# Kernel optimization log

Measured on AMD Instinct MI355X. Metric: run time of the kernel, lower is better.

The kernel has to match this reference:

```python
import jax, jax.numpy as jnp
import numpy as np

# Static dims
N = 512        # nodes
T = 8          # window_size
E = 16384      # edges per timestep
F0, H1, FP = 128, 256, 64   # feat_proj_dims
FN = 16        # noise dim
WIN = FP + FN  # WLE in_channels = 80
WH = 128       # WLE hidden
D_SSM = 1      # TLSSM d_model = d_ssm = 1 (scalar per node pair)
D_STATE = 16
D_CONV = 4
CONV_DIM = D_SSM + 2 * D_STATE          # 33
D_IN = 2 * D_SSM + 2 * D_STATE + 1      # z, xBC, dt -> 35
PRED = 1


def setup_inputs() -> dict:
    key = jax.random.key(0)
    ks = jax.random.split(key, 24)
    s = 0.05
    rn = lambda k, shp: jax.random.normal(k, shp, dtype=jnp.float32) * s
    return {
        "edge_index": jax.random.randint(ks[0], (T, 2, E), 0, N, dtype=jnp.int64),
        "edge_weight": jax.random.uniform(ks[1], (T, E), dtype=jnp.float32),
        "feats": jax.random.normal(ks[2], (T, N, F0), dtype=jnp.float32),
        "noise": jax.random.normal(ks[3], (T, N, FN), dtype=jnp.float32),
        # feat_proj MLP
        "Wp1": rn(ks[4], (F0, H1)), "bp1": jnp.zeros((H1,), jnp.float32),
        "Wp2": rn(ks[5], (H1, FP)), "bp2": jnp.zeros((FP,), jnp.float32),
        # WeightedLinkEncoder
        "wle_W1": rn(ks[6], (WIN, WH)), "wle_b1": jnp.zeros((WH,), jnp.float32),
        "wle_W2": rn(ks[7], (WH, WH)), "wle_b2": jnp.zeros((WH,), jnp.float32),
        "wle_W3": rn(ks[8], (WH, WH)), "wle_b3": jnp.zeros((WH,), jnp.float32),
        "wle_w4": rn(ks[9], (WH, 1)), "wle_b4": jnp.zeros((1,), jnp.float32),
        # TLSSM (Mamba2-style stepwise)
        "W_in": rn(ks[10], (D_SSM, D_IN)),
        "conv_w": rn(ks[11], (CONV_DIM, D_CONV)),
        "conv_b": jnp.zeros((CONV_DIM,), jnp.float32),
        "dt_bias": jnp.zeros((1,), jnp.float32),
        "A_log": jnp.zeros((1,), jnp.float32),
        "D_skip": jnp.ones((1,), jnp.float32) * s,
        "W_out": rn(ks[12], (D_SSM, D_SSM)),
    }


def _forward(edge_index, edge_weight, feats, noise,
             Wp1, bp1, Wp2, bp2,
             wle_W1, wle_b1, wle_W2, wle_b2, wle_W3, wle_b3, wle_w4, wle_b4,
             W_in, conv_w, conv_b, dt_bias, A_log, D_skip, W_out):
    # feat_proj: stacked Linear+ReLU, vectorized over timesteps
    h = jax.nn.relu(feats @ Wp1 + bp1)
    h = jax.nn.relu(h @ Wp2 + bp2)              # [T, N, FP]
    emb = jnp.concatenate([h, noise], axis=-1)

    # WeightedLinkEncoder: node MLP -> weighted sparse propagation -> edge score
    def wle(x, ei, ew):
        hh = jax.nn.relu(x @ wle_W1 + wle_b1)                       # [N, WH]
        msg = ew[:, None] * hh[ei[1]]                               # gather neighbors
        agg = jax.ops.segment_sum(msg, ei[0], num_segments=N)      # scatter-add
        h2 = jax.nn.relu((hh + agg) @ wle_W2 + wle_b2)
        ef = h2[ei[0]] * h2[ei[1]]                                 # per-edge hadamard
        s = jax.nn.relu(ef @ wle_W3 + wle_b3) @ wle_w4 + wle_b4    # [E, 1]
        return s[:, 0]

    scores = jax.vmap(wle)(emb, edge_index, edge_weight)            # [T, E]

    # SparseTensor(...).to_dense(): densify edge scores to N x N per step
    def dens(ei, s):
        return jnp.zeros((N, N), scores.dtype).at[ei[0], ei[1]].set(s)

    dense = jax.vmap(dens)(edge_index, scores).reshape(T, N * N, D_SSM)

    # TLSSM stepwise recurrence over the window, batch = N*N
    A = -jnp.exp(A_log)  # [1]

    def step(carry, xt):
        conv_state, ssm_state = carry                    # [BN,CONV_DIM,D_CONV], [BN,D_SSM,D_STATE]
        zxbcdt = xt @ W_in                               # [BN, D_IN]
        z, xBC, dt = jnp.split(zxbcdt, [D_SSM, D_SSM + CONV_DIM], axis=-1)
        conv_state = jnp.concatenate([conv_state[:, :, 1:], xBC[:, :, None]], axis=-1)
        xBC = jax.nn.silu(jnp.sum(conv_state * conv_w, axis=-1) + conv_b)
        x_, Bm, Cm = jnp.split(xBC, [D_SSM, D_SSM + D_STATE], axis=-1)
        dt = jax.nn.softplus(dt + dt_bias)               # [BN, 1]
        dA = jnp.exp(dt * A)                             # [BN, 1]
        ssm_state = ssm_state * dA[:, :, None] + (dt * x_)[:, :, None] * Bm[:, None, :]
        y = jnp.sum(ssm_state * Cm[:, None, :], axis=-1) + D_skip * x_
        y = y * jax.nn.silu(z)
        return (conv_state, ssm_state), y @ W_out

    conv0 = jnp.zeros((N * N, CONV_DIM, D_CONV), jnp.float32)
    ssm0 = jnp.zeros((N * N, D_SSM, D_STATE), jnp.float32)
    _, ys = jax.lax.scan(step, (conv0, ssm0), dense)     # [T, BN, 1]
    out = ys.reshape(T, N, N)[-PRED:]                    # pred_flag=True: last pred_size steps
    return out


def reference(edge_index, edge_weight, feats, noise,
              Wp1, bp1, Wp2, bp2,
              wle_W1, wle_b1, wle_W2, wle_b2, wle_W3, wle_b3, wle_w4, wle_b4,
              W_in, conv_w, conv_b, dt_bias, A_log, D_skip, W_out):
    return _forward(edge_index, edge_weight, feats, noise,
                    Wp1, bp1, Wp2, bp2,
                    wle_W1, wle_b1, wle_W2, wle_b2, wle_W3, wle_b3, wle_w4, wle_b4,
                    W_in, conv_w, conv_b, dt_bias, A_log, D_skip, W_out)
```

## Files before the change

### kernel.cpp

```cpp
#include <hip/hip_runtime.h>
#include <math.h>

#define Nn 512
#define Tt 8
#define Ee 16384
#define NNc (Nn*Nn)
#define TNr (Tt*Nn)
#define TE  (Tt*Ee)
#define CAP 128

typedef __bf16 bf16x8 __attribute__((ext_vector_type(8)));
typedef float  f32x4  __attribute__((ext_vector_type(4)));
union BU { uint4 q; bf16x8 v; };

__device__ __forceinline__ void dec2(float x0, float x1, unsigned &hi, unsigned &lo){
    unsigned u0 = __float_as_uint(x0), u1 = __float_as_uint(x1);
    unsigned t0 = u0 + 0x7FFFu + ((u0>>16)&1u);
    unsigned t1 = u1 + 0x7FFFu + ((u1>>16)&1u);
    hi = (t0>>16) | (t1 & 0xFFFF0000u);
    float h0 = __uint_as_float(t0 & 0xFFFF0000u);
    float h1 = __uint_as_float(t1 & 0xFFFF0000u);
    float l0 = x0 - h0, l1 = x1 - h1;
    unsigned v0 = __float_as_uint(l0), v1 = __float_as_uint(l1);
    unsigned s0 = v0 + 0x7FFFu + ((v0>>16)&1u);
    unsigned s1 = v1 + 0x7FFFu + ((v1>>16)&1u);
    lo = (s0>>16) | (s1 & 0xFFFF0000u);
}

__global__ __launch_bounds__(256) void k_pf(
    const int* __restrict__ ei, const float* __restrict__ W3,
    unsigned short* __restrict__ w3h, unsigned short* __restrict__ w3l,
    int* __restrict__ cnt, int* __restrict__ tag, float4* __restrict__ out4,
    const float* __restrict__ feats, const float* __restrict__ noise,
    const float* __restrict__ Wp1, const float* __restrict__ bp1,
    const float* __restrict__ Wp2, const float* __restrict__ bp2,
    const float* __restrict__ W1, const float* __restrict__ b1,
    float* __restrict__ hh)
{
    __shared__ float sh1[8][256];
    __shared__ float semb[8][80];
    int tid = threadIdx.x;
    if (blockIdx.x < 64){
        int e = blockIdx.x*256 + tid;
        int a = ei[7*2*Ee + e], b = ei[7*2*Ee + Ee + e];
        int cell = a*Nn + b;
#pragma unroll
        for (int t=0;t<8;++t) tag[t*NNc + cell] = 0;
        if (e < TNr) cnt[e] = 0;
        float4 z = {0.f,0.f,0.f,0.f};
#pragma unroll
        for (int q=0;q<4;++q) out4[q*16384 + e] = z;
        int i    = e & 7;
        int lane = (e>>3) & 63;
        int jt   = (e>>9) & 7;
        int kt   = e>>12;
        int k = kt*32 + (lane>>4)*8 + i;
        int j = jt*16 + (lane&15);
        float x = W3[k*128 + j];
        unsigned u = __float_as_uint(x);
        unsigned t = u + 0x7FFFu + ((u>>16)&1u);
        w3h[e] = (unsigned short)(t>>16);
        float hf = __uint_as_float(t & 0xFFFF0000u);
        float lf = x - hf;
        unsigned v = __float_as_uint(lf);
        unsigned s = v + 0x7FFFu + ((v>>16)&1u);
        w3l[e] = (unsigned short)(s>>16);
        return;
    }
    int r0 = (blockIdx.x - 64) * 8;
    if (tid < 128){
        int r = tid>>4, k = tid&15;
        semb[r][64+k] = noise[(size_t)(r0+r)*16 + k];
    }
    {
        const float* __restrict__ fr = &feats[(size_t)r0*128];
        float acc[8];
#pragma unroll
        for (int r=0;r<8;++r) acc[r]=0.f;
#pragma unroll 2
        for (int i=0;i<128;i+=4){
            float w0=Wp1[(i+0)*256+tid], w1=Wp1[(i+1)*256+tid];
            float w2=Wp1[(i+2)*256+tid], w3=Wp1[(i+3)*256+tid];
#pragma unroll
            for (int r=0;r<8;++r){
                float4 f = *(const float4*)&fr[r*128 + i];
                acc[r] += f.x*w0 + f.y*w1 + f.z*w2 + f.w*w3;
            }
        }
        float b = bp1[tid];
#pragma unroll
        for (int r=0;r<8;++r) sh1[r][tid] = fmaxf(acc[r]+b, 0.f);
    }
    __syncthreads();
    {
        int jo = tid & 63, rq = tid >> 6;
        float a0=0.f, a1=0.f;
#pragma unroll 2
        for (int i=0;i<256;i+=4){
            float w0=Wp2[(i+0)*64+jo], w1=Wp2[(i+1)*64+jo];
            float w2=Wp2[(i+2)*64+jo], w3=Wp2[(i+3)*64+jo];
            float4 f0 = *(const float4*)&sh1[rq][i];
            float4 f1 = *(const float4*)&sh1[rq+4][i];
            a0 += f0.x*w0 + f0.y*w1 + f0.z*w2 + f0.w*w3;
            a1 += f1.x*w0 + f1.y*w1 + f1.z*w2 + f1.w*w3;
        }
        float b = bp2[jo];
        semb[rq][jo]   = fmaxf(a0+b, 0.f);
        semb[rq+4][jo] = fmaxf(a1+b, 0.f);
    }
    __syncthreads();
    {
        int j = tid & 127, rh = tid >> 7;
        float a[4];
#pragma unroll
        for (int q=0;q<4;++q) a[q]=0.f;
#pragma unroll 2
        for (int i=0;i<80;i+=4){
            float w0=W1[(i+0)*128+j], w1=W1[(i+1)*128+j];
            float w2=W1[(i+2)*128+j], w3=W1[(i+3)*128+j];
#pragma unroll
            for (int q=0;q<4;++q){
                float4 f = *(const float4*)&semb[rh+2*q][i];
                a[q] += f.x*w0 + f.y*w1 + f.z*w2 + f.w*w3;
            }
        }
        float b = b1[j];
#pragma unroll
        for (int q=0;q<4;++q)
            hh[(size_t)(r0+rh+2*q)*128 + j] = fmaxf(a[q]+b, 0.f);
    }
}

__global__ __launch_bounds__(256) void k_histtag(
    const int* __restrict__ ei, const float* __restrict__ ew,
    int* __restrict__ cnt, int2* __restrict__ bucket2, int* __restrict__ tag)
{
    int g = blockIdx.x*256 + threadIdx.x;
    int t = g>>14, e = g&(Ee-1);
    int a = ei[t*2*Ee + e];
    int b = ei[t*2*Ee + Ee + e];
    int cell = t*Nn + a;
    int pos = atomicAdd(&cnt[cell], 1);
    if (pos < CAP) bucket2[(size_t)cell*CAP + pos] = make_int2(b, __float_as_int(ew[g]));
    atomicMax(&tag[t*NNc + a*Nn + b], g+1);
}

__global__ __launch_bounds__(256) void k_sw(
    const float* __restrict__ hh, const int* __restrict__ cnt,
    const int2* __restrict__ bucket2,
    const float* __restrict__ W2, const float* __restrict__ b2,
    float* __restrict__ h2)
{
    __shared__ float sx[2][128];
    int dloc = threadIdx.x >> 7;
    int ch = threadIdx.x & 127;
    int bidd = blockIdx.x*2 + dloc;
    int t = bidd >> 9;
    int n = cnt[bidd]; n = n < CAP ? n : CAP;
    const int2* __restrict__ bk = &bucket2[(size_t)bidd*CAP];
    const float* __restrict__ hht = &hh[(size_t)t*Nn*128];
    float acc = hh[(size_t)bidd*128 + ch];
    int i = 0;
    for (; i+1 < n; i += 2){
        int2 p0 = bk[i], p1 = bk[i+1];
        acc += __int_as_float(p0.y)*hht[(size_t)p0.x*128 + ch]
             + __int_as_float(p1.y)*hht[(size_t)p1.x*128 + ch];
    }
    if (i < n){
        int2 p = bk[i];
        acc += __int_as_float(p.y)*hht[(size_t)p.x*128 + ch];
    }
    sx[dloc][ch] = acc;
    __syncthreads();
    float s = 0.f;
    for (int i2=0; i2<128; i2+=4){
        float4 x = *(const float4*)&sx[dloc][i2];
        s += x.x*W2[(i2+0)*128+ch] + x.y*W2[(i2+1)*128+ch]
           + x.z*W2[(i2+2)*128+ch] + x.w*W2[(i2+3)*128+ch];
    }
    h2[(size_t)bidd*128 + ch] = fmaxf(s + b2[ch], 0.f);
}

__global__ __launch_bounds__(512) void k_edge9(
    const int* __restrict__ ei, const float* __restrict__ h2,
    const uint4* __restrict__ w3h, const uint4* __restrict__ w3l,
    const float* __restrict__ b3, const float* __restrict__ w4,
    const float* __restrict__ b4, float* __restrict__ sc)
{
    __shared__ uint4 sBh[2048];
    __shared__ uint4 sBl[2048];
    int tid = threadIdx.x;
    int bid = blockIdx.x;
#pragma unroll
    for (int q=0;q<4;++q){
        sBh[q*512+tid] = w3h[q*512+tid];
        sBl[q*512+tid] = w3l[q*512+tid];
    }
    int tb  = bid >> 6;
    int e0b = (bid & 63) * 256;
    int w   = tid >> 6, lane = tid & 63;
    int e0w = e0b + w*32;
    int r16 = lane & 15, g4 = lane >> 4;

    const int* __restrict__ eit = &ei[tb*2*Ee];
    int a0 = eit[e0w + r16],      s0 = eit[Ee + e0w + r16];
    int a1 = eit[e0w + 16 + r16], s1 = eit[Ee + e0w + 16 + r16];
    const float* __restrict__ pa0 = &h2[(size_t)(tb*Nn+a0)*128];
    const float* __restrict__ pb0 = &h2[(size_t)(tb*Nn+s0)*128];
    const float* __restrict__ pa1 = &h2[(size_t)(tb*Nn+a1)*128];
    const float* __restrict__ pb1 = &h2[(size_t)(tb*Nn+s1)*128];

    f32x4 acc0[8], acc1[8];
#pragma unroll
    for (int jt=0;jt<8;++jt){
        acc0[jt] = (f32x4){0.f,0.f,0.f,0.f};
        acc1[jt] = (f32x4){0.f,0.f,0.f,0.f};
    }

    float4 rA0,rA1,rB0,rB1,rC0,rC1,rD0,rD1;
#define LOADK(kt) { int k0=(kt)*32+g4*8; \
    rA0=*(const float4*)&pa0[k0]; rA1=*(const float4*)&pa0[k0+4]; \
    rB0=*(const float4*)&pb0[k0]; rB1=*(const float4*)&pb0[k0+4]; \
    rC0=*(const float4*)&pa1[k0]; rC1=*(const float4*)&pa1[k0+4]; \
    rD0=*(const float4*)&pb1[k0]; rD1=*(const float4*)&pb1[k0+4]; }

    BU ah0[2], al0[2], ah1[2], al1[2];
#define DECK(s) { uint4 hq,lq; \
    dec2(rA0.x*rB0.x, rA0.y*rB0.y, hq.x, lq.x); \
    dec2(rA0.z*rB0.z, rA0.w*rB0.w, hq.y, lq.y); \
    dec2(rA1.x*rB1.x, rA1.y*rB1.y, hq.z, lq.z); \
    dec2(rA1.z*rB1.z, rA1.w*rB1.w, hq.w, lq.w); \
    ah0[s].q=hq; al0[s].q=lq; \
    dec2(rC0.x*rD0.x, rC0.y*rD0.y, hq.x, lq.x); \
    dec2(rC0.z*rD0.z, rC0.w*rD0.w, hq.y, lq.y); \
    dec2(rC1.x*rD1.x, rC1.y*rD1.y, hq.z, lq.z); \
    dec2(rC1.z*rD1.z, rC1.w*rD1.w, hq.w, lq.w); \
    ah1[s].q=hq; al1[s].q=lq; }

    LOADK(0)
    DECK(0)
    __syncthreads();
#pragma unroll
    for (int kt=0;kt<4;++kt){
        if (kt < 3) LOADK(kt+1)
        const int s = kt & 1;
#pragma unroll
        for (int jt=0;jt<8;++jt){
            BU Bh, Bl;
            Bh.q = sBh[(kt*8+jt)*64 + lane];
            Bl.q = sBl[(kt*8+jt)*64 + lane];
            acc0[jt] = __builtin_amdgcn_mfma_f32_16x16x32_bf16(ah0[s].v, Bh.v, acc0[jt], 0,0,0);
            acc0[jt] = __builtin_amdgcn_mfma_f32_16x16x32_bf16(ah0[s].v, Bl.v, acc0[jt], 0,0,0);
            acc0[jt] = __builtin_amdgcn_mfma_f32_16x16x32_bf16(al0[s].v, Bh.v, acc0[jt], 0,0,0);
            acc1[jt] = __builtin_amdgcn_mfma_f32_16x16x32_bf16(ah1[s].v, Bh.v, acc1[jt], 0,0,0);
            acc1[jt] = __builtin_amdgcn_mfma_f32_16x16x32_bf16(ah1[s].v, Bl.v, acc1[jt], 0,0,0);
            acc1[jt] = __builtin_amdgcn_mfma_f32_16x16x32_bf16(al1[s].v, Bh.v, acc1[jt], 0,0,0);
        }
        if (kt < 3) DECK((kt+1)&1)
    }

    float b4v = b4[0];
    float b3v[8], w4v[8];
#pragma unroll
    for (int jt=0;jt<8;++jt){ b3v[jt] = b3[jt*16 + r16]; w4v[jt] = w4[jt*16 + r16]; }
#pragma unroll
    for (int r=0;r<4;++r){
        float p0 = 0.f, p1 = 0.f;
#pragma unroll
        for (int jt=0;jt<8;++jt){
            p0 += fmaxf(acc0[jt][r] + b3v[jt], 0.f) * w4v[jt];
            p1 += fmaxf(acc1[jt][r] + b3v[jt], 0.f) * w4v[jt];
        }
        p0 += __shfl_xor(p0,1); p0 += __shfl_xor(p0,2);
        p0 += __shfl_xor(p0,4); p0 += __shfl_xor(p0,8);
        p1 += __shfl_xor(p1,1); p1 += __shfl_xor(p1,2);
        p1 += __shfl_xor(p1,4); p1 += __shfl_xor(p1,8);
        if (r16 == 0){
            sc[(size_t)tb*Ee + e0w + g4*4 + r]      = p0 + b4v;
            sc[(size_t)tb*Ee + e0w + 16 + g4*4 + r] = p1 + b4v;
        }
    }
}

__global__ __launch_bounds__(256) void k_ssm2(
    const int* __restrict__ ei, const int* __restrict__ tag,
    const float* __restrict__ sc,
    const float* __restrict__ W_in, const float* __restrict__ conv_w,
    const float* __restrict__ conv_b, const float* __restrict__ dt_bias,
    const float* __restrict__ A_log, const float* __restrict__ D_skip,
    const float* __restrict__ W_out, float* __restrict__ out)
{
    __shared__ float scw[132], scb[33], swin[35];
    int tid = threadIdx.x;
    if (tid < 132) scw[tid] = conv_w[tid];
    if (tid < 33)  scb[tid] = conv_b[tid];
    if (tid < 35)  swin[tid] = W_in[tid];
    __syncthreads();

    int e = blockIdx.x*256 + tid;
    int a = ei[7*2*Ee + e], b = ei[7*2*Ee + Ee + e];
    int cell = a*Nn + b;
    float x[8];
#pragma unroll
    for (int t=0;t<8;++t){
        int tg = tag[t*NNc + cell];
        x[t] = (tg > 0) ? sc[tg-1] : 0.f;
    }

    float A    = -expf(A_log[0]);
    float dtb  = dt_bias[0];
    float dsk  = D_skip[0];
    float wout = W_out[0];
    float win_z = swin[0], win_dt = swin[34];

    float ssm[16];
#pragma unroll
    for (int q=0;q<16;++q) ssm[q]=0.f;
    float h0=0.f,h1=0.f,h2v=0.f;
    float y=0.f;
    for (int t=0;t<8;++t){
        float xt = x[t];
        float act[33];
#pragma unroll
        for (int c=0;c<33;++c){
            float s = h0*scw[c*4+0] + h1*scw[c*4+1] + h2v*scw[c*4+2] + xt*scw[c*4+3];
            float pre = swin[1+c]*s + scb[c];
            act[c] = pre / (1.f + expf(-pre));
        }
        float x_ = act[0];
        float dtr = xt*win_dt + dtb;
        float dt  = (dtr > 20.f) ? dtr : log1pf(expf(dtr));
        float dA  = expf(dt*A);
        float dx  = dt*x_;
        float yv = 0.f;
#pragma unroll
        for (int q=0;q<16;++q){
            ssm[q] = ssm[q]*dA + dx*act[1+q];
            yv += ssm[q]*act[17+q];
        }
        yv += dsk*x_;
        float z = xt*win_z;
        yv *= z / (1.f + expf(-z));
        y = yv;
        h0=h1; h1=h2v; h2v=xt;
    }
    out[cell] = y*wout;
}

extern "C" void kernel_launch(void* const* d_in, const int* in_sizes, int n_in,
                              void* d_out, int out_size, void* d_ws, size_t ws_size,
                              hipStream_t stream)
{
    const int*   ei    = (const int*)d_in[0];
    const float* ew    = (const float*)d_in[1];
    const float* feats = (const float*)d_in[2];
    const float* noise = (const float*)d_in[3];
    const float* Wp1=(const float*)d_in[4];  const float* bp1=(const float*)d_in[5];
    const float* Wp2=(const float*)d_in[6];  const float* bp2=(const float*)d_in[7];
    const float* W1 =(const float*)d_in[8];  const float* b1 =(const float*)d_in[9];
    const float* W2 =(const float*)d_in[10]; const float* b2 =(const float*)d_in[11];
    const float* W3 =(const float*)d_in[12]; const float* b3 =(const float*)d_in[13];
    const float* w4 =(const float*)d_in[14]; const float* b4 =(const float*)d_in[15];
    const float* W_in  =(const float*)d_in[16]; const float* conv_w=(const float*)d_in[17];
    const float* conv_b=(const float*)d_in[18]; const float* dt_bias=(const float*)d_in[19];
    const float* A_log =(const float*)d_in[20]; const float* D_skip=(const float*)d_in[21];
    const float* W_out =(const float*)d_in[22];

    float* out = (float*)d_out;
    float* ws  = (float*)d_ws;
    float* hh    = ws;
    float* h2    = hh    + 524288;
    float* sc    = h2    + 524288;
    int*   cnt   = (int*)(sc + 131072);
    int*   tag   = cnt + TNr;
    int2*  bucket2 = (int2*)(tag + 2097152);
    unsigned short* w3h = (unsigned short*)(bucket2 + (size_t)TNr*CAP);
    unsigned short* w3l = w3h + 16384;

    k_pf      <<<576, 256, 0, stream>>>(ei, W3, w3h, w3l, cnt, tag, (float4*)out,
                                        feats, noise, Wp1, bp1, Wp2, bp2, W1, b1, hh);
    k_histtag <<<TE/256, 256, 0, stream>>>(ei, ew, cnt, bucket2, tag);
    k_sw      <<<TNr/2, 256, 0, stream>>>(hh, cnt, bucket2, W2, b2, h2);
    k_edge9   <<<512, 512, 0, stream>>>(ei, h2, (const uint4*)w3h, (const uint4*)w3l,
                                        b3, w4, b4, sc);
    k_ssm2    <<<Ee/256, 256, 0, stream>>>(ei, tag, sc, W_in, conv_w, conv_b,
                                           dt_bias, A_log, D_skip, W_out, out);
}
```

Before: 105.4 us.

## Move first feature-projection layer onto split-bf16 MFMA in a separate kernel

The first projection layer (feats @ Wp1) leaves the fused per-8-row FMA kernel and becomes its own kernel. That kernel uses 16x16x32 bf16 MFMA with a hi/lo split (three MFMAs per tile) to keep near-fp32 accuracy. A prep kernel pre-splits Wp1 into MFMA-fragment-ordered bf16 halves, and the remaining layers run in a second kernel that reads h1 through the bucket workspace region. The aim is to replace the large scalar FMA cost, at the price of two extra launches, an h1 round trip through global memory, and a k_l1 grid of only 32 blocks.

Result: slower. 118.8 us (+12.6%).

```diff
diff --git a/kernel.cpp b/kernel.cpp
--- a/kernel.cpp
+++ b/kernel.cpp
@@ -27,18 +27,24 @@
     lo = (s0>>16) | (s1 & 0xFFFF0000u);
 }
 
-__global__ __launch_bounds__(256) void k_pf(
+__device__ __forceinline__ void splitw(float x, unsigned short* ph, unsigned short* pl, int idx){
+    unsigned u = __float_as_uint(x);
+    unsigned t = u + 0x7FFFu + ((u>>16)&1u);
+    ph[idx] = (unsigned short)(t>>16);
+    float hf = __uint_as_float(t & 0xFFFF0000u);
+    float lf = x - hf;
+    unsigned v = __float_as_uint(lf);
+    unsigned s = v + 0x7FFFu + ((v>>16)&1u);
+    pl[idx] = (unsigned short)(s>>16);
+}
+
+__global__ __launch_bounds__(256) void k_prep(
     const int* __restrict__ ei, const float* __restrict__ W3,
+    const float* __restrict__ Wp1,
     unsigned short* __restrict__ w3h, unsigned short* __restrict__ w3l,
-    int* __restrict__ cnt, int* __restrict__ tag, float4* __restrict__ out4,
-    const float* __restrict__ feats, const float* __restrict__ noise,
-    const float* __restrict__ Wp1, const float* __restrict__ bp1,
-    const float* __restrict__ Wp2, const float* __restrict__ bp2,
-    const float* __restrict__ W1, const float* __restrict__ b1,
-    float* __restrict__ hh)
-{
-    __shared__ float sh1[8][256];
-    __shared__ float semb[8][80];
+    unsigned short* __restrict__ p1h, unsigned short* __restrict__ p1l,
+    int* __restrict__ cnt, int* __restrict__ tag, float4* __restrict__ out4)
+{
     int tid = threadIdx.x;
     if (blockIdx.x < 64){
         int e = blockIdx.x*256 + tid;
@@ -56,40 +62,104 @@
         int kt   = e>>12;
         int k = kt*32 + (lane>>4)*8 + i;
         int j = jt*16 + (lane&15);
-        float x = W3[k*128 + j];
-        unsigned u = __float_as_uint(x);
-        unsigned t = u + 0x7FFFu + ((u>>16)&1u);
-        w3h[e] = (unsigned short)(t>>16);
-        float hf = __uint_as_float(t & 0xFFFF0000u);
-        float lf = x - hf;
-        unsigned v = __float_as_uint(lf);
-        unsigned s = v + 0x7FFFu + ((v>>16)&1u);
-        w3l[e] = (unsigned short)(s>>16);
+        splitw(W3[k*128 + j], w3h, w3l, e);
         return;
     }
-    int r0 = (blockIdx.x - 64) * 8;
+    int idx = (blockIdx.x - 64)*256 + tid;
+    int i    = idx & 7;
+    int lane = (idx>>3) & 63;
+    int jt   = (idx>>9) & 15;
+    int kt   = idx>>13;
+    int k = kt*32 + (lane>>4)*8 + i;
+    int j = jt*16 + (lane&15);
+    splitw(Wp1[k*256 + j], p1h, p1l, idx);
+}
+
+__global__ __launch_bounds__(256) void k_l1(
+    const float* __restrict__ feats, const uint4* __restrict__ p1h,
+    const uint4* __restrict__ p1l, const float* __restrict__ bp1,
+    float* __restrict__ h1)
+{
+    int tid = threadIdx.x;
+    int w = tid >> 6, lane = tid & 63;
+    int r16 = lane & 15, g4 = lane >> 4;
+    int r0w = blockIdx.x*128 + w*32;
+    const float* __restrict__ pa0 = &feats[(size_t)(r0w + r16)*128];
+    const float* __restrict__ pa1 = &feats[(size_t)(r0w + 16 + r16)*128];
+
+    f32x4 acc0[16], acc1[16];
+#pragma unroll
+    for (int jt=0;jt<16;++jt){
+        acc0[jt] = (f32x4){0.f,0.f,0.f,0.f};
+        acc1[jt] = (f32x4){0.f,0.f,0.f,0.f};
+    }
+
+#pragma unroll
+    for (int kt=0;kt<4;++kt){
+        int k0 = kt*32 + g4*8;
+        BU Ah0, Al0, Ah1, Al1;
+        {
+            float4 xa = *(const float4*)&pa0[k0], ya = *(const float4*)&pa0[k0+4];
+            uint4 hq, lq;
+            dec2(xa.x, xa.y, hq.x, lq.x);
+            dec2(xa.z, xa.w, hq.y, lq.y);
+            dec2(ya.x, ya.y, hq.z, lq.z);
+            dec2(ya.z, ya.w, hq.w, lq.w);
+            Ah0.q = hq; Al0.q = lq;
+        }
+        {
+            float4 xa = *(const float4*)&pa1[k0], ya = *(const float4*)&pa1[k0+4];
+            uint4 hq, lq;
+            dec2(xa.x, xa.y, hq.x, lq.x);
+            dec2(xa.z, xa.w, hq.y, lq.y);
+            dec2(ya.x, ya.y, hq.z, lq.z);
+            dec2(ya.z, ya.w, hq.w, lq.w);
+            Ah1.q = hq; Al1.q = lq;
+        }
+#pragma unroll
+        for (int jt=0;jt<16;++jt){
+            BU Bh, Bl;
+            Bh.q = p1h[(kt*16+jt)*64 + lane];
+            Bl.q = p1l[(kt*16+jt)*64 + lane];
+            acc0[jt] = __builtin_amdgcn_mfma_f32_16x16x32_bf16(Ah0.v, Bh.v, acc0[jt], 0,0,0);
+            acc0[jt] = __builtin_amdgcn_mfma_f32_16x16x32_bf16(Ah0.v, Bl.v, acc0[jt], 0,0,0);
+            acc0[jt] = __builtin_amdgcn_mfma_f32_16x16x32_bf16(Al0.v, Bh.v, acc0[jt], 0,0,0);
+            acc1[jt] = __builtin_amdgcn_mfma_f32_16x16x32_bf16(Ah1.v, Bh.v, acc1[jt], 0,0,0);
+            acc1[jt] = __builtin_amdgcn_mfma_f32_16x16x32_bf16(Ah1.v, Bl.v, acc1[jt], 0,0,0);
+            acc1[jt] = __builtin_amdgcn_mfma_f32_16x16x32_bf16(Al1.v, Bh.v, acc1[jt], 0,0,0);
+        }
+    }
+#pragma unroll
+    for (int jt=0;jt<16;++jt){
+        float b = bp1[jt*16 + r16];
+        int jcol = jt*16 + r16;
+#pragma unroll
+        for (int r=0;r<4;++r){
+            int row0 = r0w + g4*4 + r;
+            h1[(size_t)row0*256 + jcol]      = fmaxf(acc0[jt][r] + b, 0.f);
+            h1[(size_t)(row0+16)*256 + jcol] = fmaxf(acc1[jt][r] + b, 0.f);
+        }
+    }
+}
+
+__global__ __launch_bounds__(256) void k_l23(
+    const float* __restrict__ h1, const float* __restrict__ noise,
+    const float* __restrict__ Wp2, const float* __restrict__ bp2,
+    const float* __restrict__ W1, const float* __restrict__ b1,
+    float* __restrict__ hh)
+{
+    __shared__ float sh1[8][256];
+    __shared__ float semb[8][80];
+    int tid = threadIdx.x;
+    int r0 = blockIdx.x * 8;
+    {
+        const float4* __restrict__ src = (const float4*)&h1[(size_t)r0*256];
+        ((float4*)sh1)[tid]       = src[tid];
+        ((float4*)sh1)[256 + tid] = src[256 + tid];
+    }
     if (tid < 128){
         int r = tid>>4, k = tid&15;
         semb[r][64+k] = noise[(size_t)(r0+r)*16 + k];
-    }
-    {
-        const float* __restrict__ fr = &feats[(size_t)r0*128];
-        float acc[8];
-#pragma unroll
-        for (int r=0;r<8;++r) acc[r]=0.f;
-#pragma unroll 2
-        for (int i=0;i<128;i+=4){
-            float w0=Wp1[(i+0)*256+tid], w1=Wp1[(i+1)*256+tid];
-            float w2=Wp1[(i+2)*256+tid], w3=Wp1[(i+3)*256+tid];
-#pragma unroll
-            for (int r=0;r<8;++r){
-                float4 f = *(const float4*)&fr[r*128 + i];
-                acc[r] += f.x*w0 + f.y*w1 + f.z*w2 + f.w*w3;
-            }
-        }
-        float b = bp1[tid];
-#pragma unroll
-        for (int r=0;r<8;++r) sh1[r][tid] = fmaxf(acc[r]+b, 0.f);
     }
     __syncthreads();
     {
@@ -374,11 +444,17 @@
     int*   cnt   = (int*)(sc + 131072);
     int*   tag   = cnt + TNr;
     int2*  bucket2 = (int2*)(tag + 2097152);
+    float* h1    = (float*)bucket2;
     unsigned short* w3h = (unsigned short*)(bucket2 + (size_t)TNr*CAP);
     unsigned short* w3l = w3h + 16384;
-
-    k_pf      <<<576, 256, 0, stream>>>(ei, W3, w3h, w3l, cnt, tag, (float4*)out,
-                                        feats, noise, Wp1, bp1, Wp2, bp2, W1, b1, hh);
+    unsigned short* p1h = w3l + 16384;
+    unsigned short* p1l = p1h + 32768;
+
+    k_prep    <<<192, 256, 0, stream>>>(ei, W3, Wp1, w3h, w3l, p1h, p1l,
+                                        cnt, tag, (float4*)out);
+    k_l1      <<<32, 256, 0, stream>>>(feats, (const uint4*)p1h, (const uint4*)p1l,
+                                       bp1, h1);
+    k_l23     <<<512, 256, 0, stream>>>(h1, noise, Wp2, bp2, W1, b1, hh);
     k_histtag <<<TE/256, 256, 0, stream>>>(ei, ew, cnt, bucket2, tag);
     k_sw      <<<TNr/2, 256, 0, stream>>>(hh, cnt, bucket2, W2, b2, h2);
     k_edge9   <<<512, 512, 0, stream>>>(ei, h2, (const uint4*)w3h, (const uint4*)w3l,
```
